# Optimization experiments

Measured on AMD Instinct MI355X. Metric: run time of the kernel, lower is better.

The kernel has to match this reference:

```python
import jax, jax.numpy as jnp
import numpy as np

NY, NX = 512, 512  # grid_size[1], grid_size[0]
M = 100000
C = 64
B = 4


def setup_inputs() -> dict:
    key = jax.random.key(0)
    k1, k2, k3, k4 = jax.random.split(key, 4)
    pillar_features = jax.random.normal(k1, (M, C), dtype=jnp.float32)
    b_idx = jax.random.randint(k2, (M,), 0, B)
    z_idx = jnp.zeros((M,), dtype=jnp.int64 if jax.config.jax_enable_x64 else jnp.int32)
    y_idx = jax.random.randint(k3, (M,), 0, NY)
    x_idx = jax.random.randint(k4, (M,), 0, NX)
    coordinates = jnp.stack([b_idx, z_idx.astype(b_idx.dtype), y_idx, x_idx], axis=1)
    return {"pillar_features": pillar_features, "coordinates": coordinates, "batch_size": B}


def reference(pillar_features, coordinates, batch_size):
    # Fused batch-aware scatter: flat index = b * (NY*NX) + y * NX + x
    flat_idx = coordinates[:, 0] * (NY * NX) + coordinates[:, 2] * NX + coordinates[:, 3]
    canvas = jnp.zeros((batch_size * NY * NX, pillar_features.shape[1]),
                       dtype=pillar_features.dtype)
    canvas = canvas.at[flat_idx].set(pillar_features)
    # (B*NY*NX, C) -> (B, C, NY, NX)
    return canvas.reshape(batch_size, NY, NX, -1).transpose(0, 3, 1, 2)
```

## Files before the change

kernel.cpp:

```cpp
#include <hip/hip_runtime.h>


#define NXc 512
#define NYc 512
#define Cc  64

__global__ void __launch_bounds__(256)
winners_kernel(const int* __restrict__ coords, int* __restrict__ winner, int M) {
    int m = blockIdx.x * blockDim.x + threadIdx.x;
    if (m >= M) return;
    int4 cd = ((const int4*)coords)[m];
    int slot = cd.x * (NYc * NXc) + cd.z * NXc + cd.w;
    atomicMax(&winner[slot], m);
}

__global__ void __launch_bounds__(256)
gather_kernel(const float* __restrict__ feat, const int* __restrict__ winner,
              float* __restrict__ out) {
    int tid = blockIdx.x * blockDim.x + threadIdx.x;
    int x4 = (tid & (NXc / 4 - 1)) * 4;
    int by = tid >> 7;
    int y  = by & (NYc - 1);
    int b  = by >> 9;
    const int plane = NYc * NXc;

    int4 w = *(const int4*)(winner + b * plane + y * NXc + x4);

    float* obase = out + (size_t)(b * Cc) * plane + y * NXc + x4;

    #pragma unroll 4
    for (int cg = 0; cg < Cc / 4; ++cg) {
        float4 f0 = {0.f, 0.f, 0.f, 0.f};
        float4 f1 = f0, f2 = f0, f3 = f0;
        if (w.x >= 0) f0 = *(const float4*)(feat + (size_t)w.x * Cc + cg * 4);
        if (w.y >= 0) f1 = *(const float4*)(feat + (size_t)w.y * Cc + cg * 4);
        if (w.z >= 0) f2 = *(const float4*)(feat + (size_t)w.z * Cc + cg * 4);
        if (w.w >= 0) f3 = *(const float4*)(feat + (size_t)w.w * Cc + cg * 4);
        float4 o;
        o = make_float4(f0.x, f1.x, f2.x, f3.x);
        *(float4*)(obase + (size_t)(cg * 4 + 0) * plane) = o;
        o = make_float4(f0.y, f1.y, f2.y, f3.y);
        *(float4*)(obase + (size_t)(cg * 4 + 1) * plane) = o;
        o = make_float4(f0.z, f1.z, f2.z, f3.z);
        *(float4*)(obase + (size_t)(cg * 4 + 2) * plane) = o;
        o = make_float4(f0.w, f1.w, f2.w, f3.w);
        *(float4*)(obase + (size_t)(cg * 4 + 3) * plane) = o;
    }
}

extern "C" void kernel_launch(void* const* d_in, const int* in_sizes, int n_in,
                              void* d_out, int out_size, void* d_ws, size_t ws_size,
                              hipStream_t stream) {
    const float* feat   = (const float*)d_in[0];
    const int*   coords = (const int*)d_in[1];
    float*       out    = (float*)d_out;

    const int M = in_sizes[1] / 4;
    const int B = out_size / (Cc * NYc * NXc);

    int* winner = (int*)d_ws;
    const size_t wbytes = (size_t)B * NYc * NXc * sizeof(int);

    hipMemsetAsync(winner, 0xFF, wbytes, stream);

    winners_kernel<<<(M + 255) / 256, 256, 0, stream>>>(coords, winner, M);

    const int nthreads = B * NYc * NXc / 4;
    gather_kernel<<<nthreads / 256, 256, 0, stream>>>(feat, winner, out);
}
```

Measured before the change: 296.0 us.

## Stage occupied pillar rows in LDS before transposed output writes

Each block compacts the occupied cells it covers with an LDS atomic counter. It then loads their feature rows cooperatively and coalesced into padded shared memory, and the transpose reads from LDS instead of issuing scattered per-thread float4 global loads. Blocks with more than the capacity of occupied cells fall back to direct global reads. This adds two barriers and about 44KB of LDS per block, which may lower occupancy.

```diff
diff --git a/kernel.cpp b/kernel.cpp
--- a/kernel.cpp
+++ b/kernel.cpp
@@ -1,9 +1,11 @@
 #include <hip/hip_runtime.h>
 
 
-#define NXc 512
-#define NYc 512
-#define Cc  64
+#define NXc   512
+#define NYc   512
+#define Cc    64
+#define CAP   160
+#define ROWF  68
 
 __global__ void __launch_bounds__(256)
 winners_kernel(const int* __restrict__ coords, int* __restrict__ winner, int M) {
@@ -17,25 +19,59 @@
 __global__ void __launch_bounds__(256)
 gather_kernel(const float* __restrict__ feat, const int* __restrict__ winner,
               float* __restrict__ out) {
-    int tid = blockIdx.x * blockDim.x + threadIdx.x;
-    int x4 = (tid & (NXc / 4 - 1)) * 4;
-    int by = tid >> 7;
-    int y  = by & (NYc - 1);
-    int b  = by >> 9;
+    __shared__ float rows[CAP * ROWF];
+    __shared__ int   widxs[CAP];
+    __shared__ int   counter;
+
+    const int tid  = threadIdx.x;
+    const int gtid = blockIdx.x * 256 + tid;
+    const int x4   = (gtid & (NXc / 4 - 1)) * 4;
+    const int by   = gtid >> 7;
+    const int y    = by & (NYc - 1);
+    const int b    = by >> 9;
     const int plane = NYc * NXc;
 
+    if (tid == 0) counter = 0;
+    __syncthreads();
+
     int4 w = *(const int4*)(winner + b * plane + y * NXc + x4);
+    int cnt = (w.x >= 0) + (w.y >= 0) + (w.z >= 0) + (w.w >= 0);
+    int base = 0;
+    if (cnt) base = atomicAdd(&counter, cnt);
+
+    int rr = base;
+    int r0 = (w.x >= 0) ? rr++ : -1;
+    int r1 = (w.y >= 0) ? rr++ : -1;
+    int r2 = (w.z >= 0) ? rr++ : -1;
+    int r3 = (w.w >= 0) ? rr++ : -1;
+    if (r0 >= 0 && r0 < CAP) widxs[r0] = w.x;
+    if (r1 >= 0 && r1 < CAP) widxs[r1] = w.y;
+    if (r2 >= 0 && r2 < CAP) widxs[r2] = w.z;
+    if (r3 >= 0 && r3 < CAP) widxs[r3] = w.w;
+    __syncthreads();
+
+    const int nOcc = min(counter, CAP);
+    for (int i = tid; i < nOcc * 16; i += 256) {
+        int row = i >> 4, seg = i & 15;
+        float4 v = *(const float4*)(feat + (size_t)widxs[row] * Cc + seg * 4);
+        *(float4*)(rows + row * ROWF + seg * 4) = v;
+    }
+    __syncthreads();
 
     float* obase = out + (size_t)(b * Cc) * plane + y * NXc + x4;
 
-    #pragma unroll 4
+    #pragma unroll
     for (int cg = 0; cg < Cc / 4; ++cg) {
         float4 f0 = {0.f, 0.f, 0.f, 0.f};
         float4 f1 = f0, f2 = f0, f3 = f0;
-        if (w.x >= 0) f0 = *(const float4*)(feat + (size_t)w.x * Cc + cg * 4);
-        if (w.y >= 0) f1 = *(const float4*)(feat + (size_t)w.y * Cc + cg * 4);
-        if (w.z >= 0) f2 = *(const float4*)(feat + (size_t)w.z * Cc + cg * 4);
-        if (w.w >= 0) f3 = *(const float4*)(feat + (size_t)w.w * Cc + cg * 4);
+        if (r0 >= 0) f0 = (r0 < CAP) ? *(const float4*)(rows + r0 * ROWF + cg * 4)
+                                     : *(const float4*)(feat + (size_t)w.x * Cc + cg * 4);
+        if (r1 >= 0) f1 = (r1 < CAP) ? *(const float4*)(rows + r1 * ROWF + cg * 4)
+                                     : *(const float4*)(feat + (size_t)w.y * Cc + cg * 4);
+        if (r2 >= 0) f2 = (r2 < CAP) ? *(const float4*)(rows + r2 * ROWF + cg * 4)
+                                     : *(const float4*)(feat + (size_t)w.z * Cc + cg * 4);
+        if (r3 >= 0) f3 = (r3 < CAP) ? *(const float4*)(rows + r3 * ROWF + cg * 4)
+                                     : *(const float4*)(feat + (size_t)w.w * Cc + cg * 4);
         float4 o;
         o = make_float4(f0.x, f1.x, f2.x, f3.x);
         *(float4*)(obase + (size_t)(cg * 4 + 0) * plane) = o;
```

Result: slower. 303.1 us (+2.4%).
